# Optimization experiments

Measured on AMD Instinct MI355X. Metric: run time of the kernel, lower is better.

## Reference

```python
import jax, jax.numpy as jnp
import numpy as np

U, I, D, L, NNZ = 8000, 16000, 64, 2, 768000
N = U + I


def setup_inputs() -> dict:
    key = jax.random.key(0)
    ks = jax.random.split(key, 10)
    return {
        "user_indices": jnp.arange(U, dtype=jnp.int64) if jax.config.jax_enable_x64 else jnp.arange(U, dtype=jnp.int32),
        "item_indices": jnp.arange(I, dtype=jnp.int32),
        "adj_rows": jax.random.randint(ks[0], (NNZ,), 0, N, dtype=jnp.int32),
        "adj_cols": jax.random.randint(ks[1], (NNZ,), 0, N, dtype=jnp.int32),
        "adj_vals": jax.random.uniform(ks[2], (NNZ,), dtype=jnp.float32),
        "user_emb": 0.1 * jax.random.normal(ks[3], (U, D), dtype=jnp.float32),
        "item_emb": 0.1 * jax.random.normal(ks[4], (I, D), dtype=jnp.float32),
        "gc_W": 0.05 * jax.random.normal(ks[5], (L, D, D), dtype=jnp.float32),
        "gc_b": jnp.zeros((L, D), dtype=jnp.float32),
        "bi_W": 0.05 * jax.random.normal(ks[6], (L, D, D), dtype=jnp.float32),
        "bi_b": jnp.zeros((L, D), dtype=jnp.float32),
    }


def reference(user_indices, item_indices, adj_rows, adj_cols, adj_vals,
              user_emb, item_emb, gc_W, gc_b, bi_W, bi_b):
    # embedding lookups + concat -> ego embeddings [N, D]
    ego = jnp.concatenate([user_emb[user_indices], item_emb[item_indices]], axis=0)
    n_nodes = ego.shape[0]
    all_embeddings = [ego]
    n_layers = gc_W.shape[0]
    for l in range(n_layers):
        # sparse.mm(adj, ego): gather neighbor rows, weight, scatter-add to rows
        side = jax.ops.segment_sum(adj_vals[:, None] * ego[adj_cols], adj_rows,
                                   num_segments=n_nodes)  # [N, D]
        sum_emb = jax.nn.leaky_relu(side @ gc_W[l].T + gc_b[l], negative_slope=0.01)
        bi_emb = jax.nn.leaky_relu((ego * side) @ bi_W[l].T + bi_b[l], negative_slope=0.01)
        ego = sum_emb + bi_emb
        all_embeddings.append(ego)
    all_emb = jnp.concatenate(all_embeddings, axis=1)  # [N, D*(L+1)]
    n_users = user_indices.shape[0]
    u_g = all_emb[:n_users]
    i_g = all_emb[n_users:]
    scores = u_g @ i_g.T  # [U, I]
    return jax.nn.log_softmax(scores, axis=1)
```

## Files before the change

kernel.cpp:

```cpp
#include <hip/hip_runtime.h>
#include <hip/hip_bf16.h>
#include <math.h>

#define NU   8000
#define NI   16000
#define NN   24000
#define DD   64
#define NL   2
#define NNZS 768000
#define KD   192
#define NCH  25
#define ACHUNK 640
#define CTILES 5
#define RBLK 63
#define CBLK 125
#define SCH  24

typedef __attribute__((ext_vector_type(8))) short  short8;
typedef __attribute__((ext_vector_type(4))) float  f32x4;

__device__ __forceinline__ unsigned short f2bf(float x) {
    union { float f; unsigned int u; } v; v.f = x;
    unsigned int r = v.u + 0x7fff + ((v.u >> 16) & 1);
    return (unsigned short)(r >> 16);
}
__device__ __forceinline__ float bf2f(unsigned short u) {
    union { unsigned int u; float f; } v; v.u = ((unsigned int)u) << 16;
    return v.f;
}

__device__ __forceinline__ int bslot(int nf, int kt, int g, int r16) {
    return ((((kt * 8 + nf) * 4 + g) * 16) + r16) ^ ((g + 4 * kt) & 7);
}

__global__ void k_concat(const int* __restrict__ uidx, const int* __restrict__ iidx,
                         const float* __restrict__ ue, const float* __restrict__ ie,
                         const float* __restrict__ gcW, const float* __restrict__ biW,
                         unsigned short* __restrict__ allemb,
                         unsigned short* __restrict__ wbf, int* __restrict__ cnt) {
    int t = blockIdx.x * blockDim.x + threadIdx.x;
    if (t < NN) cnt[t] = 0;
    if (t < NL * DD * DD) {
        wbf[t] = f2bf(gcW[t]);
        wbf[NL * DD * DD + t] = f2bf(biW[t]);
    }
    if (t >= NN * DD) return;
    int n = t >> 6, d = t & 63;
    float v = (n < NU) ? ue[uidx[n] * DD + d] : ie[iidx[n - NU] * DD + d];
    allemb[(size_t)n * KD + d] = f2bf(v);
}

__global__ void k_hist(const int* __restrict__ rows, int* __restrict__ cnt) {
    int e = blockIdx.x * blockDim.x + threadIdx.x;
    if (e < NNZS) atomicAdd(&cnt[rows[e]], 1);
}

__global__ __launch_bounds__(1024) void k_scan1(const int* __restrict__ cnt,
                                                int* __restrict__ rp, int* __restrict__ btot) {
    __shared__ int wsum[16];
    int tid = threadIdx.x, lane = tid & 63, wid = tid >> 6;
    int i = blockIdx.x * 1024 + tid;
    int v = (i < NN) ? cnt[i] : 0;
    int x = v;
#pragma unroll
    for (int off = 1; off < 64; off <<= 1) {
        int t = __shfl_up(x, off, 64);
        if (lane >= off) x += t;
    }
    if (lane == 63) wsum[wid] = x;
    __syncthreads();
    if (tid < 16) {
        int y = wsum[tid];
#pragma unroll
        for (int off = 1; off < 16; off <<= 1) {
            int t = __shfl_up(y, off, 64);
            if (tid >= off) y += t;
        }
        wsum[tid] = y;
    }
    __syncthreads();
    int incl = x + (wid ? wsum[wid - 1] : 0);
    if (i < NN) rp[i + 1] = incl;
    if (tid == 0) btot[blockIdx.x] = wsum[15];
}

__global__ void k_scan2(const int* __restrict__ btot, int* __restrict__ boff) {
    int tid = threadIdx.x;
    int v = (tid < SCH) ? btot[tid] : 0;
    int x = v;
#pragma unroll
    for (int off = 1; off < 32; off <<= 1) {
        int t = __shfl_up(x, off, 64);
        if (tid >= off) x += t;
    }
    if (tid < SCH) boff[tid] = x - v;
}

__global__ __launch_bounds__(1024) void k_scan3(const int* __restrict__ cnt,
                                                const int* __restrict__ boff,
                                                int* __restrict__ rp, int* __restrict__ wp) {
    int i = blockIdx.x * 1024 + threadIdx.x;
    if (i == 0) rp[0] = 0;
    if (i >= NN) return;
    int g = rp[i + 1] + boff[blockIdx.x];
    rp[i + 1] = g;
    wp[i] = g - cnt[i];
}

__global__ void k_scatter(const int* __restrict__ rows, const int* __restrict__ cols,
                          const float* __restrict__ vals, int* __restrict__ wp,
                          int2* __restrict__ edat) {
    int e = blockIdx.x * blockDim.x + threadIdx.x;
    if (e >= NNZS) return;
    int r = rows[e];
    int pos = atomicAdd(&wp[r], 1);
    edat[pos] = make_int2(cols[e], __float_as_int(vals[e]));
}

__global__ void k_spmm_csr(const int* __restrict__ rp, const int2* __restrict__ edat,
                           const unsigned short* __restrict__ feat, float* __restrict__ side) {
    int lane = threadIdx.x & 63;
    int wave = (blockIdx.x * blockDim.x + threadIdx.x) >> 6;
    int nw   = (gridDim.x * blockDim.x) >> 6;
    for (int r = wave; r < NN; r += nw) {
        int e0 = rp[r], e1 = rp[r + 1];
        float acc = 0.f;
        int e = e0;
        for (; e + 8 <= e1; e += 8) {
            int2 d[8];
#pragma unroll
            for (int j = 0; j < 8; ++j) d[j] = edat[e + j];
#pragma unroll
            for (int j = 0; j < 8; ++j)
                acc = fmaf(__int_as_float(d[j].y), bf2f(feat[(size_t)d[j].x * KD + lane]), acc);
        }
        for (; e < e1; ++e) {
            int2 d = edat[e];
            acc = fmaf(__int_as_float(d.y), bf2f(feat[(size_t)d.x * KD + lane]), acc);
        }
        side[(size_t)r * DD + lane] = acc;
    }
}

__global__ __launch_bounds__(256) void k_dense(const float* __restrict__ side,
                        unsigned short* __restrict__ allemb, int l,
                        const unsigned short* __restrict__ wg_bf,
                        const unsigned short* __restrict__ wb_bf,
                        const float* __restrict__ gcb, const float* __restrict__ bib) {
    int lane = threadIdx.x & 63;
    int wave = threadIdx.x >> 6;
    int n0 = (blockIdx.x * 4 + wave) * 16;
    int nrow = lane & 15;
    int kofs = (lane >> 4) * 8;
    const unsigned short* feat = allemb + l * DD;

    short8 bg[4][2], bb[4][2];
#pragma unroll
    for (int nf = 0; nf < 4; ++nf)
#pragma unroll
        for (int kt = 0; kt < 2; ++kt) {
            bg[nf][kt] = *(const short8*)(wg_bf + (nf * 16 + nrow) * DD + kt * 32 + kofs);
            bb[nf][kt] = *(const short8*)(wb_bf + (nf * 16 + nrow) * DD + kt * 32 + kofs);
        }

    short8 a1[2], a2[2];
    const float* sp = side + (size_t)(n0 + nrow) * DD;
    const unsigned short* ep = feat + (size_t)(n0 + nrow) * KD;
#pragma unroll
    for (int kt = 0; kt < 2; ++kt) {
        int o = kt * 32 + kofs;
#pragma unroll
        for (int j = 0; j < 8; ++j) {
            float s = sp[o + j];
            float e = bf2f(ep[o + j]);
            a1[kt][j] = (short)f2bf(s);
            a2[kt][j] = (short)f2bf(e * s);
        }
    }

    f32x4 acc1[4], acc2[4];
#pragma unroll
    for (int nf = 0; nf < 4; ++nf) { acc1[nf] = (f32x4){0,0,0,0}; acc2[nf] = (f32x4){0,0,0,0}; }
#pragma unroll
    for (int nf = 0; nf < 4; ++nf)
#pragma unroll
        for (int kt = 0; kt < 2; ++kt) {
            acc1[nf] = __builtin_amdgcn_mfma_f32_16x16x32_bf16(a1[kt], bg[nf][kt], acc1[nf], 0, 0, 0);
            acc2[nf] = __builtin_amdgcn_mfma_f32_16x16x32_bf16(a2[kt], bb[nf][kt], acc2[nf], 0, 0, 0);
        }

    int g = lane >> 4;
#pragma unroll
    for (int nf = 0; nf < 4; ++nf) {
        int o = nf * 16 + nrow;
        float b1 = gcb[o], b2 = bib[o];
#pragma unroll
        for (int r = 0; r < 4; ++r) {
            int node = n0 + g * 4 + r;
            float v1 = acc1[nf][r] + b1;
            float v2 = acc2[nf][r] + b2;
            v1 = v1 > 0.f ? v1 : 0.01f * v1;
            v2 = v2 > 0.f ? v2 : 0.01f * v2;
            allemb[(size_t)node * KD + (l + 1) * DD + o] = f2bf(v1 + v2);
        }
    }
}

__global__ __launch_bounds__(256) void k_lse_part(const unsigned short* __restrict__ allemb,
                                                  float* __restrict__ pm, float* __restrict__ ps) {
    __shared__ short8 Bs[3072];
    int id = blockIdx.x;
    int rowblk = id % RBLK;
    int chunk  = id / RBLK;
    int tid = threadIdx.x;
    int lane = tid & 63;
    int wave = tid >> 6;
    int r0 = rowblk * 128 + wave * 32;
    int c0 = chunk * ACHUNK;
    const unsigned short* A = allemb;
    const unsigned short* B = allemb + (size_t)NU * KD;
    int kofs = (lane >> 4) * 8;
    int g = lane >> 4;

    short8 a[2][6];
#pragma unroll
    for (int mi = 0; mi < 2; ++mi) {
        int ar = r0 + mi * 16 + (lane & 15);
        if (ar >= NU) ar = NU - 1;
#pragma unroll
        for (int kt = 0; kt < 6; ++kt)
            a[mi][kt] = *(const short8*)(A + (size_t)ar * KD + kt * 32 + kofs);
    }

    float m[2][4], s[2][4];
#pragma unroll
    for (int mi = 0; mi < 2; ++mi)
#pragma unroll
        for (int r = 0; r < 4; ++r) { m[mi][r] = -INFINITY; s[mi][r] = 0.f; }

    for (int t = 0; t < CTILES; ++t) {
        const unsigned short* Bt = B + (size_t)(c0 + t * 128) * KD;
        __syncthreads();
#pragma unroll
        for (int i = 0; i < 12; ++i) {
            int mm = i * 256 + tid;
            int r = mm / 24, c = mm - r * 24;
            int kt = c >> 2, gg = c & 3;
            Bs[bslot(r >> 4, kt, gg, r & 15)] = *(const short8*)(Bt + (size_t)r * KD + c * 8);
        }
        __syncthreads();

        f32x4 acc[2][8];
#pragma unroll
        for (int mi = 0; mi < 2; ++mi)
#pragma unroll
            for (int nf = 0; nf < 8; ++nf) acc[mi][nf] = (f32x4){0.f, 0.f, 0.f, 0.f};
#pragma unroll
        for (int nf = 0; nf < 8; ++nf)
#pragma unroll
            for (int kt = 0; kt < 6; ++kt) {
                short8 b = Bs[bslot(nf, kt, g, lane & 15)];
                acc[0][nf] = __builtin_amdgcn_mfma_f32_16x16x32_bf16(a[0][kt], b, acc[0][nf], 0, 0, 0);
                acc[1][nf] = __builtin_amdgcn_mfma_f32_16x16x32_bf16(a[1][kt], b, acc[1][nf], 0, 0, 0);
            }
#pragma unroll
        for (int mi = 0; mi < 2; ++mi)
#pragma unroll
            for (int r = 0; r < 4; ++r) {
                float lm = acc[mi][0][r];
#pragma unroll
                for (int nf = 1; nf < 8; ++nf) lm = fmaxf(lm, acc[mi][nf][r]);
                float nm = fmaxf(m[mi][r], lm);
                float p = 0.f;
#pragma unroll
                for (int nf = 0; nf < 8; ++nf) p += __expf(acc[mi][nf][r] - nm);
                s[mi][r] = s[mi][r] * __expf(m[mi][r] - nm) + p;
                m[mi][r] = nm;
            }
    }
#pragma unroll
    for (int mi = 0; mi < 2; ++mi)
#pragma unroll
        for (int r = 0; r < 4; ++r) {
            float mm = m[mi][r], ss = s[mi][r];
#pragma unroll
            for (int off = 1; off < 16; off <<= 1) {
                float om = __shfl_xor(mm, off, 64);
                float os = __shfl_xor(ss, off, 64);
                float nm = fmaxf(mm, om);
                ss = ss * __expf(mm - nm) + os * __expf(om - nm);
                mm = nm;
            }
            m[mi][r] = mm; s[mi][r] = ss;
        }
    if ((lane & 15) == 0) {
#pragma unroll
        for (int mi = 0; mi < 2; ++mi)
#pragma unroll
            for (int r = 0; r < 4; ++r) {
                int row = r0 + mi * 16 + g * 4 + r;
                if (row < NU) {
                    pm[chunk * NU + row] = m[mi][r];
                    ps[chunk * NU + row] = s[mi][r];
                }
            }
    }
}

__global__ void k_lse_comb(const float* __restrict__ pm, const float* __restrict__ ps,
                           float* __restrict__ lse) {
    int r = blockIdx.x * blockDim.x + threadIdx.x;
    if (r >= NU) return;
    float m = -INFINITY;
    for (int c = 0; c < NCH; ++c) m = fmaxf(m, pm[c * NU + r]);
    float s = 0.f;
    for (int c = 0; c < NCH; ++c) s += ps[c * NU + r] * __expf(pm[c * NU + r] - m);
    lse[r] = m + __logf(s);
}

__global__ __launch_bounds__(256) void k_out(const unsigned short* __restrict__ allemb,
                                             const float* __restrict__ lse, float* __restrict__ out) {
    __shared__ short8 Bs[3072];
    int id = blockIdx.x;
    int rowblk = id / CBLK;
    int colblk = id % CBLK;
    int tid = threadIdx.x;
    int lane = tid & 63;
    int wave = tid >> 6;
    int r0 = rowblk * 128 + wave * 32;
    int c0 = colblk * 128;
    const unsigned short* A = allemb;
    const unsigned short* B = allemb + (size_t)NU * KD;
    int kofs = (lane >> 4) * 8;
    int g = lane >> 4;

    const unsigned short* Bt = B + (size_t)c0 * KD;
#pragma unroll
    for (int i = 0; i < 12; ++i) {
        int mm = i * 256 + tid;
        int r = mm / 24, c = mm - r * 24;
        int kt = c >> 2, gg = c & 3;
        Bs[bslot(r >> 4, kt, gg, r & 15)] = *(const short8*)(Bt + (size_t)r * KD + c * 8);
    }

    short8 a[2][6];
#pragma unroll
    for (int mi = 0; mi < 2; ++mi) {
        int ar = r0 + mi * 16 + (lane & 15);
        if (ar >= NU) ar = NU - 1;
#pragma unroll
        for (int kt = 0; kt < 6; ++kt)
            a[mi][kt] = *(const short8*)(A + (size_t)ar * KD + kt * 32 + kofs);
    }
    float l4[2][4];
#pragma unroll
    for (int mi = 0; mi < 2; ++mi)
#pragma unroll
        for (int r = 0; r < 4; ++r) {
            int row = r0 + mi * 16 + g * 4 + r;
            l4[mi][r] = lse[row >= NU ? NU - 1 : row];
        }
    __syncthreads();

    f32x4 acc[2][8];
#pragma unroll
    for (int mi = 0; mi < 2; ++mi)
#pragma unroll
        for (int nf = 0; nf < 8; ++nf) acc[mi][nf] = (f32x4){0.f, 0.f, 0.f, 0.f};
#pragma unroll
    for (int nf = 0; nf < 8; ++nf)
#pragma unroll
        for (int kt = 0; kt < 6; ++kt) {
            short8 b = Bs[bslot(nf, kt, g, lane & 15)];
            acc[0][nf] = __builtin_amdgcn_mfma_f32_16x16x32_bf16(a[0][kt], b, acc[0][nf], 0, 0, 0);
            acc[1][nf] = __builtin_amdgcn_mfma_f32_16x16x32_bf16(a[1][kt], b, acc[1][nf], 0, 0, 0);
        }
    __syncthreads();

    float* tilef = (float*)Bs;
    float* tW = tilef + wave * 16 * 132;
#pragma unroll
    for (int mi = 0; mi < 2; ++mi) {
        int rowbase = r0 + mi * 16;
#pragma unroll
        for (int nf = 0; nf < 8; ++nf)
#pragma unroll
            for (int r = 0; r < 4; ++r)
                tW[(g * 4 + r) * 132 + nf * 16 + (lane & 15)] = acc[mi][nf][r] - l4[mi][r];
#pragma unroll
        for (int it = 0; it < 8; ++it) {
            int idx = it * 64 + lane;
            int rr = idx >> 5;
            int cc = (idx & 31) * 4;
            int row = rowbase + rr;
            if (row < NU) {
                f32x4 v = *(const f32x4*)&tW[rr * 132 + cc];
                __builtin_nontemporal_store(v, (f32x4*)&out[(size_t)row * NI + c0 + cc]);
            }
        }
    }
}

extern "C" void kernel_launch(void* const* d_in, const int* in_sizes, int n_in,
                              void* d_out, int out_size, void* d_ws, size_t ws_size,
                              hipStream_t stream) {
    const int*   uidx = (const int*)d_in[0];
    const int*   iidx = (const int*)d_in[1];
    const int*   arow = (const int*)d_in[2];
    const int*   acol = (const int*)d_in[3];
    const float* aval = (const float*)d_in[4];
    const float* ue   = (const float*)d_in[5];
    const float* ie   = (const float*)d_in[6];
    const float* gcW  = (const float*)d_in[7];
    const float* gcb  = (const float*)d_in[8];
    const float* biW  = (const float*)d_in[9];
    const float* bib  = (const float*)d_in[10];
    float* out = (float*)d_out;

    char* w = (char*)d_ws;
    unsigned short* allemb = (unsigned short*)w;  w += (size_t)NN * KD * sizeof(unsigned short);
    float* side = (float*)w;                      w += (size_t)NN * DD * sizeof(float);
    float* pm  = (float*)w;                       w += (size_t)NCH * NU * sizeof(float);
    float* ps  = (float*)w;                       w += (size_t)NCH * NU * sizeof(float);
    float* lse = (float*)w;                       w += (size_t)NU * sizeof(float);
    unsigned short* wbf = (unsigned short*)w;     w += (size_t)2 * NL * DD * DD * sizeof(unsigned short);
    int* cnt   = (int*)w;                         w += (size_t)NN * sizeof(int);
    int* rp    = (int*)w;                         w += (size_t)(NN + 4) * sizeof(int);
    int* wp    = (int*)w;                         w += (size_t)NN * sizeof(int);
    int* btot  = (int*)w;                         w += 32 * sizeof(int);
    int* boff  = (int*)w;                         w += 32 * sizeof(int);
    int2* edat = (int2*)w;                        w += (size_t)NNZS * sizeof(int2);

    unsigned short* wg_bf = wbf;
    unsigned short* wb_bf = wbf + NL * DD * DD;

    k_concat<<<(NN * DD + 255) / 256, 256, 0, stream>>>(uidx, iidx, ue, ie, gcW, biW,
                                                        allemb, wbf, cnt);

    k_hist<<<(NNZS + 255) / 256, 256, 0, stream>>>(arow, cnt);
    k_scan1<<<SCH, 1024, 0, stream>>>(cnt, rp, btot);
    k_scan2<<<1, 64, 0, stream>>>(btot, boff);
    k_scan3<<<SCH, 1024, 0, stream>>>(cnt, boff, rp, wp);
    k_scatter<<<(NNZS + 255) / 256, 256, 0, stream>>>(arow, acol, aval, wp, edat);

    for (int l = 0; l < NL; ++l) {
        k_spmm_csr<<<3000, 256, 0, stream>>>(rp, edat, allemb + l * DD, side);
        k_dense<<<NN / 64, 256, 0, stream>>>(side, allemb, l,
                                             wg_bf + l * DD * DD, wb_bf + l * DD * DD,
                                             gcb + l * DD, bib + l * DD);
    }

    k_lse_part<<<RBLK * NCH, 256, 0, stream>>>(allemb, pm, ps);
    k_lse_comb<<<(NU + 255) / 256, 256, 0, stream>>>(pm, ps, lse);
    k_out<<<RBLK * CBLK, 256, 0, stream>>>(allemb, lse, out);
}
```

Before: 485.6 us.

## Stage B tiles via direct global-to-LDS loads, merge scans, chunk output kernel

Replaces the register-staged B tile copy into LDS with global_load_lds direct transfers in both the lse partial and output kernels, with the swizzled layout precomputed per source address. Replaces the three-kernel prefix scan with a single-block scan that handles 24 elements per thread. Restructures k_out so each block loops over five column tiles of a chunk, giving fewer, longer-lived blocks that reuse their A fragments and lse values. The trade-off is less parallelism in the output kernel and a serial single-block scan.

```diff
diff --git a/kernel.cpp b/kernel.cpp
--- a/kernel.cpp
+++ b/kernel.cpp
@@ -13,8 +13,6 @@
 #define ACHUNK 640
 #define CTILES 5
 #define RBLK 63
-#define CBLK 125
-#define SCH  24
 
 typedef __attribute__((ext_vector_type(8))) short  short8;
 typedef __attribute__((ext_vector_type(4))) float  f32x4;
@@ -31,6 +29,26 @@
 
 __device__ __forceinline__ int bslot(int nf, int kt, int g, int r16) {
     return ((((kt * 8 + nf) * 4 + g) * 16) + r16) ^ ((g + 4 * kt) & 7);
+}
+
+__device__ __forceinline__ void gload16(const unsigned short* g, void* lds) {
+    __builtin_amdgcn_global_load_lds(
+        (const __attribute__((address_space(1))) unsigned int*)g,
+        (__attribute__((address_space(3))) unsigned int*)lds,
+        16, 0, 0);
+}
+
+__device__ __forceinline__ void stage_B(const unsigned short* __restrict__ Bt,
+                                        short8* Bs, int tid) {
+    int wofs = tid & ~63;
+#pragma unroll
+    for (int i = 0; i < 12; ++i) {
+        int s = i * 256 + tid;
+        int kt = s >> 9, nf = (s >> 6) & 7, gg = (s >> 4) & 3;
+        int r16 = (s & 15) ^ ((gg + 4 * kt) & 7);
+        const unsigned short* src = Bt + (size_t)(nf * 16 + r16) * KD + (kt * 4 + gg) * 8;
+        gload16(src, (void*)(Bs + i * 256 + wofs));
+    }
 }
 
 __global__ void k_concat(const int* __restrict__ uidx, const int* __restrict__ iidx,
@@ -55,13 +73,21 @@
     if (e < NNZS) atomicAdd(&cnt[rows[e]], 1);
 }
 
-__global__ __launch_bounds__(1024) void k_scan1(const int* __restrict__ cnt,
-                                                int* __restrict__ rp, int* __restrict__ btot) {
+__global__ __launch_bounds__(1024) void k_scan(const int* __restrict__ cnt,
+                                               int* __restrict__ rp, int* __restrict__ wp) {
     __shared__ int wsum[16];
+    const int PT = 24;
     int tid = threadIdx.x, lane = tid & 63, wid = tid >> 6;
-    int i = blockIdx.x * 1024 + tid;
-    int v = (i < NN) ? cnt[i] : 0;
-    int x = v;
+    int base = tid * PT;
+    int v[PT];
+    int sum = 0;
+#pragma unroll
+    for (int j = 0; j < PT; ++j) {
+        int i = base + j;
+        v[j] = (i < NN) ? cnt[i] : 0;
+        sum += v[j];
+    }
+    int x = sum;
 #pragma unroll
     for (int off = 1; off < 64; off <<= 1) {
         int t = __shfl_up(x, off, 64);
@@ -79,32 +105,17 @@
         wsum[tid] = y;
     }
     __syncthreads();
-    int incl = x + (wid ? wsum[wid - 1] : 0);
-    if (i < NN) rp[i + 1] = incl;
-    if (tid == 0) btot[blockIdx.x] = wsum[15];
-}
-
-__global__ void k_scan2(const int* __restrict__ btot, int* __restrict__ boff) {
-    int tid = threadIdx.x;
-    int v = (tid < SCH) ? btot[tid] : 0;
-    int x = v;
-#pragma unroll
-    for (int off = 1; off < 32; off <<= 1) {
-        int t = __shfl_up(x, off, 64);
-        if (tid >= off) x += t;
-    }
-    if (tid < SCH) boff[tid] = x - v;
-}
-
-__global__ __launch_bounds__(1024) void k_scan3(const int* __restrict__ cnt,
-                                                const int* __restrict__ boff,
-                                                int* __restrict__ rp, int* __restrict__ wp) {
-    int i = blockIdx.x * 1024 + threadIdx.x;
-    if (i == 0) rp[0] = 0;
-    if (i >= NN) return;
-    int g = rp[i + 1] + boff[blockIdx.x];
-    rp[i + 1] = g;
-    wp[i] = g - cnt[i];
+    int run = (x - sum) + (wid ? wsum[wid - 1] : 0);
+    if (tid == 0) rp[0] = 0;
+#pragma unroll
+    for (int j = 0; j < PT; ++j) {
+        int i = base + j;
+        if (i < NN) {
+            run += v[j];
+            rp[i + 1] = run;
+            wp[i] = run - v[j];
+        }
+    }
 }
 
 __global__ void k_scatter(const int* __restrict__ rows, const int* __restrict__ cols,
@@ -239,15 +250,8 @@
         for (int r = 0; r < 4; ++r) { m[mi][r] = -INFINITY; s[mi][r] = 0.f; }
 
     for (int t = 0; t < CTILES; ++t) {
-        const unsigned short* Bt = B + (size_t)(c0 + t * 128) * KD;
         __syncthreads();
-#pragma unroll
-        for (int i = 0; i < 12; ++i) {
-            int mm = i * 256 + tid;
-            int r = mm / 24, c = mm - r * 24;
-            int kt = c >> 2, gg = c & 3;
-            Bs[bslot(r >> 4, kt, gg, r & 15)] = *(const short8*)(Bt + (size_t)r * KD + c * 8);
-        }
+        stage_B(B + (size_t)(c0 + t * 128) * KD, Bs, tid);
         __syncthreads();
 
         f32x4 acc[2][8];
@@ -322,27 +326,17 @@
                                              const float* __restrict__ lse, float* __restrict__ out) {
     __shared__ short8 Bs[3072];
     int id = blockIdx.x;
-    int rowblk = id / CBLK;
-    int colblk = id % CBLK;
+    int chunk  = id % NCH;
+    int rowblk = id / NCH;
     int tid = threadIdx.x;
     int lane = tid & 63;
     int wave = tid >> 6;
     int r0 = rowblk * 128 + wave * 32;
-    int c0 = colblk * 128;
     const unsigned short* A = allemb;
     const unsigned short* B = allemb + (size_t)NU * KD;
     int kofs = (lane >> 4) * 8;
     int g = lane >> 4;
 
-    const unsigned short* Bt = B + (size_t)c0 * KD;
-#pragma unroll
-    for (int i = 0; i < 12; ++i) {
-        int mm = i * 256 + tid;
-        int r = mm / 24, c = mm - r * 24;
-        int kt = c >> 2, gg = c & 3;
-        Bs[bslot(r >> 4, kt, gg, r & 15)] = *(const short8*)(Bt + (size_t)r * KD + c * 8);
-    }
-
     short8 a[2][6];
 #pragma unroll
     for (int mi = 0; mi < 2; ++mi) {
@@ -360,42 +354,49 @@
             int row = r0 + mi * 16 + g * 4 + r;
             l4[mi][r] = lse[row >= NU ? NU - 1 : row];
         }
-    __syncthreads();
-
-    f32x4 acc[2][8];
-#pragma unroll
-    for (int mi = 0; mi < 2; ++mi)
-#pragma unroll
-        for (int nf = 0; nf < 8; ++nf) acc[mi][nf] = (f32x4){0.f, 0.f, 0.f, 0.f};
-#pragma unroll
-    for (int nf = 0; nf < 8; ++nf)
-#pragma unroll
-        for (int kt = 0; kt < 6; ++kt) {
-            short8 b = Bs[bslot(nf, kt, g, lane & 15)];
-            acc[0][nf] = __builtin_amdgcn_mfma_f32_16x16x32_bf16(a[0][kt], b, acc[0][nf], 0, 0, 0);
-            acc[1][nf] = __builtin_amdgcn_mfma_f32_16x16x32_bf16(a[1][kt], b, acc[1][nf], 0, 0, 0);
-        }
-    __syncthreads();
 
     float* tilef = (float*)Bs;
     float* tW = tilef + wave * 16 * 132;
-#pragma unroll
-    for (int mi = 0; mi < 2; ++mi) {
-        int rowbase = r0 + mi * 16;
+
+    for (int t = 0; t < CTILES; ++t) {
+        int c0 = chunk * ACHUNK + t * 128;
+        __syncthreads();
+        stage_B(B + (size_t)c0 * KD, Bs, tid);
+        __syncthreads();
+
+        f32x4 acc[2][8];
+#pragma unroll
+        for (int mi = 0; mi < 2; ++mi)
+#pragma unroll
+            for (int nf = 0; nf < 8; ++nf) acc[mi][nf] = (f32x4){0.f, 0.f, 0.f, 0.f};
 #pragma unroll
         for (int nf = 0; nf < 8; ++nf)
 #pragma unroll
-            for (int r = 0; r < 4; ++r)
-                tW[(g * 4 + r) * 132 + nf * 16 + (lane & 15)] = acc[mi][nf][r] - l4[mi][r];
-#pragma unroll
-        for (int it = 0; it < 8; ++it) {
-            int idx = it * 64 + lane;
-            int rr = idx >> 5;
-            int cc = (idx & 31) * 4;
-            int row = rowbase + rr;
-            if (row < NU) {
-                f32x4 v = *(const f32x4*)&tW[rr * 132 + cc];
-                __builtin_nontemporal_store(v, (f32x4*)&out[(size_t)row * NI + c0 + cc]);
+            for (int kt = 0; kt < 6; ++kt) {
+                short8 b = Bs[bslot(nf, kt, g, lane & 15)];
+                acc[0][nf] = __builtin_amdgcn_mfma_f32_16x16x32_bf16(a[0][kt], b, acc[0][nf], 0, 0, 0);
+                acc[1][nf] = __builtin_amdgcn_mfma_f32_16x16x32_bf16(a[1][kt], b, acc[1][nf], 0, 0, 0);
+            }
+        __syncthreads();
+
+#pragma unroll
+        for (int mi = 0; mi < 2; ++mi) {
+            int rowbase = r0 + mi * 16;
+#pragma unroll
+            for (int nf = 0; nf < 8; ++nf)
+#pragma unroll
+                for (int r = 0; r < 4; ++r)
+                    tW[(g * 4 + r) * 132 + nf * 16 + (lane & 15)] = acc[mi][nf][r] - l4[mi][r];
+#pragma unroll
+            for (int it = 0; it < 8; ++it) {
+                int idx = it * 64 + lane;
+                int rr = idx >> 5;
+                int cc = (idx & 31) * 4;
+                int row = rowbase + rr;
+                if (row < NU) {
+                    f32x4 v = *(const f32x4*)&tW[rr * 132 + cc];
+                    __builtin_nontemporal_store(v, (f32x4*)&out[(size_t)row * NI + c0 + cc]);
+                }
             }
         }
     }
@@ -427,8 +428,6 @@
     int* cnt   = (int*)w;                         w += (size_t)NN * sizeof(int);
     int* rp    = (int*)w;                         w += (size_t)(NN + 4) * sizeof(int);
     int* wp    = (int*)w;                         w += (size_t)NN * sizeof(int);
-    int* btot  = (int*)w;                         w += 32 * sizeof(int);
-    int* boff  = (int*)w;                         w += 32 * sizeof(int);
     int2* edat = (int2*)w;                        w += (size_t)NNZS * sizeof(int2);
 
     unsigned short* wg_bf = wbf;
@@ -438,9 +437,7 @@
                                                         allemb, wbf, cnt);
 
     k_hist<<<(NNZS + 255) / 256, 256, 0, stream>>>(arow, cnt);
-    k_scan1<<<SCH, 1024, 0, stream>>>(cnt, rp, btot);
-    k_scan2<<<1, 64, 0, stream>>>(btot, boff);
-    k_scan3<<<SCH, 1024, 0, stream>>>(cnt, boff, rp, wp);
+    k_scan<<<1, 1024, 0, stream>>>(cnt, rp, wp);
     k_scatter<<<(NNZS + 255) / 256, 256, 0, stream>>>(arow, acol, aval, wp, edat);
 
     for (int l = 0; l < NL; ++l) {
@@ -452,5 +449,5 @@
 
     k_lse_part<<<RBLK * NCH, 256, 0, stream>>>(allemb, pm, ps);
     k_lse_comb<<<(NU + 255) / 256, 256, 0, stream>>>(pm, ps, lse);
-    k_out<<<RBLK * CBLK, 256, 0, stream>>>(allemb, lse, out);
-}
+    k_out<<<RBLK * NCH, 256, 0, stream>>>(allemb, lse, out);
+}
```

Measured after the change: 521.1 us. +7.3%, slower.
